# Performance work log

Hardware: AMD Instinct MI355X
Metric: run time of the kernel (lower is better)

Reference implementation:

```python
import jax, jax.numpy as jnp
import numpy as np

N_M = 100000  # musicians
N_T = 100000  # tracks
E = 400000
D = 128


def _sage(x_src, x_dst, edge, W_l, b_l, W_r, n_dst):
    """PyG SAGEConv: lin_l(mean_{j in N(i)} x_src[j]) + lin_r(x_dst[i])."""
    src, dst = edge[0], edge[1]
    msg = x_src[src]                                   # [E, D] gather
    agg = jax.ops.segment_sum(msg, dst, num_segments=n_dst)
    cnt = jax.ops.segment_sum(jnp.ones((edge.shape[1],), x_src.dtype), dst,
                              num_segments=n_dst)
    agg = agg / jnp.maximum(cnt, 1.0)[:, None]         # mean aggregation
    return agg @ W_l.T + b_l + x_dst @ W_r.T


def setup_inputs() -> dict:
    key = jax.random.key(0)
    ks = jax.random.split(key, 7)
    scale = 0.05
    return {
        "x_m": jax.random.normal(ks[0], (N_M, D), jnp.float32),
        "x_t": jax.random.normal(ks[1], (N_T, D), jnp.float32),
        "Wl": jax.random.normal(ks[2], (3, 2, D, D), jnp.float32) * scale,
        "bl": jnp.zeros((3, 2, D), jnp.float32),
        "Wr": jax.random.normal(ks[3], (3, 2, D, D), jnp.float32) * scale,
        "edge_mt": jax.random.randint(ks[4], (2, E), 0, N_T, jnp.int32).astype(jnp.int64),
        "edge_tm": jax.random.randint(ks[5], (2, E), 0, N_M, jnp.int32).astype(jnp.int64),
    }


def reference(x_m, x_t, Wl, bl, Wr, edge_mt, edge_tm):
    # 3 HeteroConv(SAGEConv) layers; dropout=0.0 is identity.
    for layer in range(3):
        # edge type 0: musician -plays_on-> track  (dst = track)
        new_t = _sage(x_m, x_t, edge_mt, Wl[layer, 0], bl[layer, 0], Wr[layer, 0], N_T)
        # edge type 1: track -features-> musician  (dst = musician)
        new_m = _sage(x_t, x_m, edge_tm, Wl[layer, 1], bl[layer, 1], Wr[layer, 1], N_M)
        if layer < 2:
            new_m = jax.nn.relu(new_m)
            new_t = jax.nn.relu(new_t)
        x_m, x_t = new_m, new_t
    return x_m, x_t
```

## Files before the change

### kernel.cpp

```cpp
#include <hip/hip_runtime.h>
#include <hip/hip_bf16.h>

typedef __bf16 bf16_t;
typedef __attribute__((ext_vector_type(4))) __bf16 bf16x4;
typedef __attribute__((ext_vector_type(8))) __bf16 bf16x8;
typedef __attribute__((ext_vector_type(4))) float f32x4;

#define DIM 128

__device__ __forceinline__ void gl_lds16(const void* g, void* l) {
    __builtin_amdgcn_global_load_lds(
        (const __attribute__((address_space(1))) unsigned int*)g,
        (__attribute__((address_space(3))) unsigned int*)l, 16, 0, 0);
}

__global__ void prep_weights(const float* __restrict__ Wl, const float* __restrict__ Wr,
                             bf16_t* __restrict__ Wc) {
    int idx = blockIdx.x * blockDim.x + threadIdx.x;
    if (idx >= 6 * 128 * 256) return;
    int k = idx & 255;
    int n = (idx >> 8) & 127;
    int s = idx >> 15;
    float v;
    if (k < 128) v = Wl[((size_t)s * 128 + n) * 128 + k];
    else         v = Wr[((size_t)s * 128 + n) * 128 + (k - 128)];
    Wc[idx] = (bf16_t)v;
}

__global__ void count_edges2(const int* __restrict__ dA, int* __restrict__ cA,
                             const int* __restrict__ dB, int* __restrict__ cB, int E) {
    int i = blockIdx.x * blockDim.x + threadIdx.x;
    if (i < E) atomicAdd(&cA[dA[i]], 1);
    else if (i < 2 * E) atomicAdd(&cB[dB[i - E]], 1);
}

__global__ __launch_bounds__(256) void scan_local(const int* __restrict__ cnt,
                                                  int* __restrict__ partial,
                                                  int* __restrict__ blocksum, int M) {
    __shared__ int sdata[256];
    int i = blockIdx.x * 256 + threadIdx.x;
    int v = (i < M) ? cnt[i] : 0;
    sdata[threadIdx.x] = v;
    __syncthreads();
    for (int off = 1; off < 256; off <<= 1) {
        int t = (threadIdx.x >= off) ? sdata[threadIdx.x - off] : 0;
        __syncthreads();
        sdata[threadIdx.x] += t;
        __syncthreads();
    }
    int incl = sdata[threadIdx.x];
    if (i < M) partial[i] = incl - v;
    if (threadIdx.x == 255) blocksum[blockIdx.x] = incl;
}

__global__ __launch_bounds__(256) void scan_blocks(int* __restrict__ blocksum, int NB) {
    __shared__ int sdata[256];
    __shared__ int running;
    if (threadIdx.x == 0) running = 0;
    __syncthreads();
    for (int base = 0; base < NB; base += 256) {
        int i = base + threadIdx.x;
        int v = (i < NB) ? blocksum[i] : 0;
        sdata[threadIdx.x] = v;
        __syncthreads();
        for (int off = 1; off < 256; off <<= 1) {
            int t = (threadIdx.x >= off) ? sdata[threadIdx.x - off] : 0;
            __syncthreads();
            sdata[threadIdx.x] += t;
            __syncthreads();
        }
        int incl = sdata[threadIdx.x];
        int r = running;
        __syncthreads();
        if (i < NB) blocksum[i] = incl - v + r;
        if (threadIdx.x == 0) running = r + sdata[255];
        __syncthreads();
    }
}

__global__ void add_offsets(const int* __restrict__ partial, const int* __restrict__ blocksum,
                            int* __restrict__ rowstart, int* __restrict__ cursor, int M) {
    int i = blockIdx.x * blockDim.x + threadIdx.x;
    if (i < M) {
        int rs = partial[i] + blocksum[i >> 8];
        rowstart[i] = rs;
        cursor[i] = rs;
    }
}

__global__ void bin_edges2(const int* __restrict__ sA, const int* __restrict__ dA,
                           int* __restrict__ curA, int* __restrict__ csrA,
                           const int* __restrict__ sB, const int* __restrict__ dB,
                           int* __restrict__ curB, int* __restrict__ csrB, int E) {
    int e = blockIdx.x * blockDim.x + threadIdx.x;
    if (e < E) {
        int d = dA[e];
        int pos = atomicAdd(&curA[d], 1);
        csrA[pos] = sA[e];
    } else if (e < 2 * E) {
        int i = e - E;
        int d = dB[i];
        int pos = atomicAdd(&curB[d], 1);
        csrB[pos] = sB[i];
    }
}

__global__ __launch_bounds__(256) void gather2(
    const float* __restrict__ xsA, const int* __restrict__ rsA,
    const int* __restrict__ cnA, const int* __restrict__ csA,
    bf16_t* __restrict__ agA, int MA,
    const float* __restrict__ xsB, const int* __restrict__ rsB,
    const int* __restrict__ cnB, const int* __restrict__ csB,
    bf16_t* __restrict__ agB, int MB) {
    int gw   = (blockIdx.x * 256 + threadIdx.x) >> 6;
    int lane = threadIdx.x & 63;
    int half = lane >> 5;
    int l32  = lane & 31;
    int side = gw & 1;
    int d    = (gw >> 1) * 2 + half;
    const float* xs; const int *rs, *cn, *cs; bf16_t* ag; int M;
    if (side == 0) { xs = xsA; rs = rsA; cn = cnA; cs = csA; ag = agA; M = MA; }
    else           { xs = xsB; rs = rsB; cn = cnB; cs = csB; ag = agB; M = MB; }
    if (d >= M) return;

    int start = rs[d];
    int n = cn[d];
    float4 acc0 = {0.f, 0.f, 0.f, 0.f};
    float4 acc1 = {0.f, 0.f, 0.f, 0.f};
    int k = 0;
    for (; k + 1 < n; k += 2) {
        int s0 = cs[start + k];
        int s1 = cs[start + k + 1];
        float4 v0 = ((const float4*)(xs + (size_t)s0 * DIM))[l32];
        float4 v1 = ((const float4*)(xs + (size_t)s1 * DIM))[l32];
        acc0.x += v0.x; acc0.y += v0.y; acc0.z += v0.z; acc0.w += v0.w;
        acc1.x += v1.x; acc1.y += v1.y; acc1.z += v1.z; acc1.w += v1.w;
    }
    if (k < n) {
        int s = cs[start + k];
        float4 v = ((const float4*)(xs + (size_t)s * DIM))[l32];
        acc0.x += v.x; acc0.y += v.y; acc0.z += v.z; acc0.w += v.w;
    }
    float invn = 1.0f / (float)max(n, 1);
    bf16x4 r;
    r[0] = (bf16_t)((acc0.x + acc1.x) * invn);
    r[1] = (bf16_t)((acc0.y + acc1.y) * invn);
    r[2] = (bf16_t)((acc0.z + acc1.z) * invn);
    r[3] = (bf16_t)((acc0.w + acc1.w) * invn);
    *(bf16x4*)(ag + (size_t)d * DIM + l32 * 4) = r;
}

#define GTILE   32
#define A0BYTES 8192
#define A1BYTES 16384
#define LDSBUF  (A0BYTES + A1BYTES)

template <bool RELU>
__global__ __launch_bounds__(256, 3) void gemm2(
    const bf16_t* __restrict__ A0a, const float* __restrict__ A1a,
    const bf16_t* __restrict__ Wca, const float* __restrict__ ba,
    float* __restrict__ oa, int Ma,
    const bf16_t* __restrict__ A0b, const float* __restrict__ A1b,
    const bf16_t* __restrict__ Wcb, const float* __restrict__ bb,
    float* __restrict__ ob, int Mb) {
    __shared__ char smem[2 * LDSBUF];
    const int tid  = threadIdx.x;
    const int wid  = tid >> 6;
    const int lane = tid & 63;
    const int quad = lane >> 4;
    const int l16  = lane & 15;

    const int side = blockIdx.x & 1;
    const int t0   = blockIdx.x >> 1;
    const int gs   = gridDim.x >> 1;

    const bf16_t* A0; const float* A1; const bf16_t* Wc; const float* bias; float* out; int M;
    if (side == 0) { A0 = A0a; A1 = A1a; Wc = Wca; bias = ba; out = oa; M = Ma; }
    else           { A0 = A0b; A1 = A1b; Wc = Wcb; bias = bb; out = ob; M = Mb; }
    const int nt = (M + GTILE - 1) / GTILE;
    if (t0 >= nt) return;

    bf16x8 breg[2][8];
#pragma unroll
    for (int ct = 0; ct < 2; ++ct)
#pragma unroll
        for (int kt = 0; kt < 8; ++kt)
            breg[ct][kt] = *(const bf16x8*)(
                Wc + (size_t)(wid * 32 + ct * 16 + l16) * 256 + kt * 32 + quad * 8);

    const float bcol0 = bias[wid * 32 + l16];
    const float bcol1 = bias[wid * 32 + 16 + l16];
    const int sw = l16 & 7;

    int a0row[2], a0sc[2];
#pragma unroll
    for (int c = 0; c < 2; ++c) {
        int o  = wid * 2048 + c * 1024 + lane * 16;
        int row = o >> 8;
        int ch  = (o >> 4) & 15;
        a0row[c] = row;
        a0sc[c]  = (ch ^ (row & 7)) * 8;
    }
    int a1row[4], a1sc[4];
#pragma unroll
    for (int c = 0; c < 4; ++c) {
        int o  = wid * 4096 + c * 1024 + lane * 16;
        int row = o >> 9;
        int ch  = (o >> 4) & 31;
        a1row[c] = row;
        a1sc[c]  = (ch ^ (row & 7)) * 4;
    }

    auto STAGE = [&](int b, int t) {
        const int r0 = t * GTILE;
        char* base = smem + b * LDSBUF;
#pragma unroll
        for (int c = 0; c < 2; ++c) {
            int grow = r0 + a0row[c]; if (grow >= M) grow = M - 1;
            gl_lds16(A0 + (size_t)grow * DIM + a0sc[c],
                     base + wid * 2048 + c * 1024);
        }
#pragma unroll
        for (int c = 0; c < 4; ++c) {
            int grow = r0 + a1row[c]; if (grow >= M) grow = M - 1;
            gl_lds16(A1 + (size_t)grow * DIM + a1sc[c],
                     base + A0BYTES + wid * 4096 + c * 1024);
        }
    };

    auto COMPUTE = [&](int b, int t) {
        const int r0 = t * GTILE;
        const char* a0base = smem + b * LDSBUF;
        const char* a1base = a0base + A0BYTES;
        f32x4 acc[2][2];
#pragma unroll
        for (int rt = 0; rt < 2; ++rt) {
            acc[rt][0] = (f32x4){0.f, 0.f, 0.f, 0.f};
            acc[rt][1] = (f32x4){0.f, 0.f, 0.f, 0.f};
        }
#pragma unroll
        for (int rt = 0; rt < 2; ++rt) {
            const int row = rt * 16 + l16;
            bf16x8 alo[4];
#pragma unroll
            for (int kt = 0; kt < 4; ++kt)
                alo[kt] = *(const bf16x8*)(a0base + row * 256 + ((kt * 4 + quad) ^ sw) * 16);
#pragma unroll
            for (int kt = 0; kt < 4; ++kt) {
                acc[rt][0] = __builtin_amdgcn_mfma_f32_16x16x32_bf16(alo[kt], breg[0][kt], acc[rt][0], 0, 0, 0);
                acc[rt][1] = __builtin_amdgcn_mfma_f32_16x16x32_bf16(alo[kt], breg[1][kt], acc[rt][1], 0, 0, 0);
            }
#pragma unroll
            for (int kt = 0; kt < 4; ++kt) {
                const int cc = kt * 8 + quad * 2;
                float4 x0 = *(const float4*)(a1base + row * 512 + ((cc)     ^ sw) * 16);
                float4 x1 = *(const float4*)(a1base + row * 512 + ((cc + 1) ^ sw) * 16);
                bf16x8 ah;
                ah[0] = (bf16_t)x0.x; ah[1] = (bf16_t)x0.y;
                ah[2] = (bf16_t)x0.z; ah[3] = (bf16_t)x0.w;
                ah[4] = (bf16_t)x1.x; ah[5] = (bf16_t)x1.y;
                ah[6] = (bf16_t)x1.z; ah[7] = (bf16_t)x1.w;
                acc[rt][0] = __builtin_amdgcn_mfma_f32_16x16x32_bf16(ah, breg[0][kt + 4], acc[rt][0], 0, 0, 0);
                acc[rt][1] = __builtin_amdgcn_mfma_f32_16x16x32_bf16(ah, breg[1][kt + 4], acc[rt][1], 0, 0, 0);
            }
        }
#pragma unroll
        for (int ct = 0; ct < 2; ++ct) {
            const int col = wid * 32 + ct * 16 + l16;
            const float bv = ct ? bcol1 : bcol0;
#pragma unroll
            for (int rt = 0; rt < 2; ++rt)
#pragma unroll
                for (int r = 0; r < 4; ++r) {
                    int row = r0 + rt * 16 + quad * 4 + r;
                    if (row < M) {
                        float v = acc[rt][ct][r] + bv;
                        if (RELU) v = fmaxf(v, 0.f);
                        out[(size_t)row * DIM + col] = v;
                    }
                }
        }
    };

    STAGE(0, t0);
    int bufi = 0;
    for (int t = t0; t < nt; t += gs, bufi ^= 1) {
        const int nxt = t + gs;
        if (nxt < nt) {
            STAGE(bufi ^ 1, nxt);
            asm volatile("s_waitcnt vmcnt(6)" ::: "memory");
        } else {
            asm volatile("s_waitcnt vmcnt(0)" ::: "memory");
        }
        __builtin_amdgcn_s_barrier();
        COMPUTE(bufi, t);
        __builtin_amdgcn_s_barrier();
        __builtin_amdgcn_sched_barrier(0);
    }
}

extern "C" void kernel_launch(void* const* d_in, const int* in_sizes, int n_in,
                              void* d_out, int out_size, void* d_ws, size_t ws_size,
                              hipStream_t stream) {
    const float* x_m = (const float*)d_in[0];
    const float* x_t = (const float*)d_in[1];
    const float* Wl  = (const float*)d_in[2];
    const float* bl  = (const float*)d_in[3];
    const float* Wr  = (const float*)d_in[4];
    const int* e_mt  = (const int*)d_in[5];
    const int* e_tm  = (const int*)d_in[6];

    const int Mm = in_sizes[0] / DIM;
    const int Mt = in_sizes[1] / DIM;
    const int E  = in_sizes[5] / 2;
    const int NBt = (Mt + 255) / 256;
    const int NBm = (Mm + 255) / 256;

    float* out_m = (float*)d_out;
    float* out_t = (float*)d_out + (size_t)Mm * DIM;

    char* ws = (char*)d_ws;
    size_t off = 0;
    auto alloc = [&](size_t bytes) -> void* {
        void* p = ws + off;
        off += (bytes + 255) & ~(size_t)255;
        return p;
    };
    float*  xm2    = (float*)alloc((size_t)Mm * DIM * 4);
    float*  xt2    = (float*)alloc((size_t)Mt * DIM * 4);
    bf16_t* aggT   = (bf16_t*)alloc((size_t)Mt * DIM * 2);
    bf16_t* aggM   = (bf16_t*)alloc((size_t)Mm * DIM * 2);
    int*    cnt_t  = (int*)alloc((size_t)Mt * 4);
    int*    cnt_m  = (int*)alloc((size_t)Mm * 4);
    int*    rs_t   = (int*)alloc((size_t)Mt * 4);
    int*    rs_m   = (int*)alloc((size_t)Mm * 4);
    int*    cur_tb = (int*)alloc((size_t)Mt * 4);
    int*    cur_mb = (int*)alloc((size_t)Mm * 4);
    int*    partial= (int*)alloc((size_t)((Mm > Mt) ? Mm : Mt) * 4);
    int*    bsum   = (int*)alloc((size_t)((NBt > NBm) ? NBt : NBm) * 4);
    int*    csr_t  = (int*)alloc((size_t)E * 4);
    int*    csr_m  = (int*)alloc((size_t)E * 4);
    bf16_t* Wc     = (bf16_t*)alloc((size_t)6 * 128 * 256 * 2);

    hipMemsetAsync(cnt_t, 0, (size_t)Mt * 4, stream);
    hipMemsetAsync(cnt_m, 0, (size_t)Mm * 4, stream);
    prep_weights<<<(6 * 128 * 256 + 255) / 256, 256, 0, stream>>>(Wl, Wr, Wc);
    count_edges2<<<(2 * E + 255) / 256, 256, 0, stream>>>(e_mt + E, cnt_t, e_tm + E, cnt_m, E);

    scan_local<<<NBt, 256, 0, stream>>>(cnt_t, partial, bsum, Mt);
    scan_blocks<<<1, 256, 0, stream>>>(bsum, NBt);
    add_offsets<<<NBt, 256, 0, stream>>>(partial, bsum, rs_t, cur_tb, Mt);

    scan_local<<<NBm, 256, 0, stream>>>(cnt_m, partial, bsum, Mm);
    scan_blocks<<<1, 256, 0, stream>>>(bsum, NBm);
    add_offsets<<<NBm, 256, 0, stream>>>(partial, bsum, rs_m, cur_mb, Mm);

    bin_edges2<<<(2 * E + 255) / 256, 256, 0, stream>>>(e_mt, e_mt + E, cur_tb, csr_t,
                                                        e_tm, e_tm + E, cur_mb, csr_m, E);

    const int wT = (Mt + 1) / 2, wM = (Mm + 1) / 2;
    const int gwaves = 2 * ((wT > wM) ? wT : wM);
    const int gblocks = (gwaves + 3) / 4;

    int GG = 768;
    {
        int ntT = (Mt + GTILE - 1) / GTILE, ntM = (Mm + GTILE - 1) / GTILE;
        int need = 2 * ((ntT > ntM) ? ntT : ntM);
        if (GG > need) GG = need;
        GG &= ~1;
        if (GG < 2) GG = 2;
    }

    const float* cm = x_m;
    const float* ct = x_t;
    for (int layer = 0; layer < 3; ++layer) {
        float *nxt_m, *nxt_t;
        if (layer == 1) { nxt_m = xm2;   nxt_t = xt2;   }
        else            { nxt_m = out_m; nxt_t = out_t; }
        const float* biasT = bl + ((size_t)layer * 2 + 0) * DIM;
        const float* biasM = bl + ((size_t)layer * 2 + 1) * DIM;
        const bf16_t* WcT = Wc + ((size_t)layer * 2 + 0) * 128 * 256;
        const bf16_t* WcM = Wc + ((size_t)layer * 2 + 1) * 128 * 256;

        gather2<<<gblocks, 256, 0, stream>>>(cm, rs_t, cnt_t, csr_t, aggT, Mt,
                                             ct, rs_m, cnt_m, csr_m, aggM, Mm);
        if (layer < 2)
            gemm2<true ><<<GG, 256, 0, stream>>>(aggT, ct, WcT, biasT, nxt_t, Mt,
                                                 aggM, cm, WcM, biasM, nxt_m, Mm);
        else
            gemm2<false><<<GG, 256, 0, stream>>>(aggT, ct, WcT, biasT, nxt_t, Mt,
                                                 aggM, cm, WcM, biasM, nxt_m, Mm);

        cm = nxt_m;
        ct = nxt_t;
    }
}
```

Measured before the change: 594.5 us.

## Merge CSR preprocessing launches and batch 8 neighbor gathers per iteration

Combines weight prep with edge counting, and runs the two scans and offset passes for both edge types in single launches. This cuts the preprocessing kernel count from eight to four and removes serialization between them, at the cost of separate partial and blocksum buffers per edge type. The aggregation loop now issues 8 index loads and 8 row gathers per iteration, with clamped indices and zero weights for the tail. This raises memory-level parallelism but adds redundant loads for low-degree nodes, which are common here at an average degree of about 4.

```diff
diff --git a/kernel.cpp b/kernel.cpp
--- a/kernel.cpp
+++ b/kernel.cpp
@@ -14,31 +14,40 @@
         (__attribute__((address_space(3))) unsigned int*)l, 16, 0, 0);
 }
 
-__global__ void prep_weights(const float* __restrict__ Wl, const float* __restrict__ Wr,
-                             bf16_t* __restrict__ Wc) {
-    int idx = blockIdx.x * blockDim.x + threadIdx.x;
-    if (idx >= 6 * 128 * 256) return;
-    int k = idx & 255;
-    int n = (idx >> 8) & 127;
-    int s = idx >> 15;
-    float v;
-    if (k < 128) v = Wl[((size_t)s * 128 + n) * 128 + k];
-    else         v = Wr[((size_t)s * 128 + n) * 128 + (k - 128)];
-    Wc[idx] = (bf16_t)v;
-}
-
-__global__ void count_edges2(const int* __restrict__ dA, int* __restrict__ cA,
-                             const int* __restrict__ dB, int* __restrict__ cB, int E) {
-    int i = blockIdx.x * blockDim.x + threadIdx.x;
-    if (i < E) atomicAdd(&cA[dA[i]], 1);
-    else if (i < 2 * E) atomicAdd(&cB[dB[i - E]], 1);
-}
-
-__global__ __launch_bounds__(256) void scan_local(const int* __restrict__ cnt,
-                                                  int* __restrict__ partial,
-                                                  int* __restrict__ blocksum, int M) {
+__global__ void prep_count(const float* __restrict__ Wl, const float* __restrict__ Wr,
+                           bf16_t* __restrict__ Wc,
+                           const int* __restrict__ dA, int* __restrict__ cA,
+                           const int* __restrict__ dB, int* __restrict__ cB,
+                           int E, int PB) {
+    int blk = blockIdx.x;
+    if (blk < PB) {
+        int idx = blk * 256 + threadIdx.x;
+        if (idx >= 6 * 128 * 256) return;
+        int k = idx & 255;
+        int n = (idx >> 8) & 127;
+        int s = idx >> 15;
+        float v;
+        if (k < 128) v = Wl[((size_t)s * 128 + n) * 128 + k];
+        else         v = Wr[((size_t)s * 128 + n) * 128 + (k - 128)];
+        Wc[idx] = (bf16_t)v;
+    } else {
+        int i = (blk - PB) * 256 + threadIdx.x;
+        if (i < E) atomicAdd(&cA[dA[i]], 1);
+        else if (i < 2 * E) atomicAdd(&cB[dB[i - E]], 1);
+    }
+}
+
+__global__ __launch_bounds__(256) void scan_local2(
+    const int* __restrict__ cntA, int* __restrict__ partA, int* __restrict__ bsumA,
+    int MA, int NBA,
+    const int* __restrict__ cntB, int* __restrict__ partB, int* __restrict__ bsumB,
+    int MB) {
+    int blk = blockIdx.x;
+    const int* cnt; int* partial; int* blocksum; int M; int b;
+    if (blk < NBA) { cnt = cntA; partial = partA; blocksum = bsumA; M = MA; b = blk; }
+    else           { cnt = cntB; partial = partB; blocksum = bsumB; M = MB; b = blk - NBA; }
     __shared__ int sdata[256];
-    int i = blockIdx.x * 256 + threadIdx.x;
+    int i = b * 256 + threadIdx.x;
     int v = (i < M) ? cnt[i] : 0;
     sdata[threadIdx.x] = v;
     __syncthreads();
@@ -50,10 +59,13 @@
     }
     int incl = sdata[threadIdx.x];
     if (i < M) partial[i] = incl - v;
-    if (threadIdx.x == 255) blocksum[blockIdx.x] = incl;
-}
-
-__global__ __launch_bounds__(256) void scan_blocks(int* __restrict__ blocksum, int NB) {
+    if (threadIdx.x == 255) blocksum[b] = incl;
+}
+
+__global__ __launch_bounds__(256) void scan_blocks2(int* __restrict__ bsA, int NA,
+                                                    int* __restrict__ bsB, int NBcnt) {
+    int* blocksum = blockIdx.x ? bsB : bsA;
+    int NB = blockIdx.x ? NBcnt : NA;
     __shared__ int sdata[256];
     __shared__ int running;
     if (threadIdx.x == 0) running = 0;
@@ -78,9 +90,16 @@
     }
 }
 
-__global__ void add_offsets(const int* __restrict__ partial, const int* __restrict__ blocksum,
-                            int* __restrict__ rowstart, int* __restrict__ cursor, int M) {
-    int i = blockIdx.x * blockDim.x + threadIdx.x;
+__global__ __launch_bounds__(256) void add_offsets2(
+    const int* __restrict__ pA, const int* __restrict__ bsA,
+    int* __restrict__ rsA, int* __restrict__ curA, int MA, int NBA,
+    const int* __restrict__ pB, const int* __restrict__ bsB,
+    int* __restrict__ rsB, int* __restrict__ curB, int MB) {
+    int blk = blockIdx.x;
+    const int *partial, *blocksum; int *rowstart, *cursor; int M, b;
+    if (blk < NBA) { partial = pA; blocksum = bsA; rowstart = rsA; cursor = curA; M = MA; b = blk; }
+    else           { partial = pB; blocksum = bsB; rowstart = rsB; cursor = curB; M = MB; b = blk - NBA; }
+    int i = b * 256 + threadIdx.x;
     if (i < M) {
         int rs = partial[i] + blocksum[i >> 8];
         rowstart[i] = rs;
@@ -127,19 +146,26 @@
     int n = cn[d];
     float4 acc0 = {0.f, 0.f, 0.f, 0.f};
     float4 acc1 = {0.f, 0.f, 0.f, 0.f};
-    int k = 0;
-    for (; k + 1 < n; k += 2) {
-        int s0 = cs[start + k];
-        int s1 = cs[start + k + 1];
-        float4 v0 = ((const float4*)(xs + (size_t)s0 * DIM))[l32];
-        float4 v1 = ((const float4*)(xs + (size_t)s1 * DIM))[l32];
-        acc0.x += v0.x; acc0.y += v0.y; acc0.z += v0.z; acc0.w += v0.w;
-        acc1.x += v1.x; acc1.y += v1.y; acc1.z += v1.z; acc1.w += v1.w;
-    }
-    if (k < n) {
-        int s = cs[start + k];
-        float4 v = ((const float4*)(xs + (size_t)s * DIM))[l32];
-        acc0.x += v.x; acc0.y += v.y; acc0.z += v.z; acc0.w += v.w;
+    for (int k = 0; k < n; k += 8) {
+        int sv[8];
+#pragma unroll
+        for (int j = 0; j < 8; ++j) {
+            int kk = k + j;
+            sv[j] = cs[start + min(kk, n - 1)];
+        }
+        float4 vv[8];
+#pragma unroll
+        for (int j = 0; j < 8; ++j)
+            vv[j] = ((const float4*)(xs + (size_t)sv[j] * DIM))[l32];
+#pragma unroll
+        for (int j = 0; j < 8; j += 2) {
+            float w0 = (k + j     < n) ? 1.f : 0.f;
+            float w1 = (k + j + 1 < n) ? 1.f : 0.f;
+            acc0.x += vv[j].x * w0; acc0.y += vv[j].y * w0;
+            acc0.z += vv[j].z * w0; acc0.w += vv[j].w * w0;
+            acc1.x += vv[j + 1].x * w1; acc1.y += vv[j + 1].y * w1;
+            acc1.z += vv[j + 1].z * w1; acc1.w += vv[j + 1].w * w1;
+        }
     }
     float invn = 1.0f / (float)max(n, 1);
     bf16x4 r;
@@ -336,25 +362,26 @@
     int*    rs_m   = (int*)alloc((size_t)Mm * 4);
     int*    cur_tb = (int*)alloc((size_t)Mt * 4);
     int*    cur_mb = (int*)alloc((size_t)Mm * 4);
-    int*    partial= (int*)alloc((size_t)((Mm > Mt) ? Mm : Mt) * 4);
-    int*    bsum   = (int*)alloc((size_t)((NBt > NBm) ? NBt : NBm) * 4);
+    int*    part_t = (int*)alloc((size_t)Mt * 4);
+    int*    part_m = (int*)alloc((size_t)Mm * 4);
+    int*    bsum_t = (int*)alloc((size_t)NBt * 4);
+    int*    bsum_m = (int*)alloc((size_t)NBm * 4);
     int*    csr_t  = (int*)alloc((size_t)E * 4);
     int*    csr_m  = (int*)alloc((size_t)E * 4);
     bf16_t* Wc     = (bf16_t*)alloc((size_t)6 * 128 * 256 * 2);
 
     hipMemsetAsync(cnt_t, 0, (size_t)Mt * 4, stream);
     hipMemsetAsync(cnt_m, 0, (size_t)Mm * 4, stream);
-    prep_weights<<<(6 * 128 * 256 + 255) / 256, 256, 0, stream>>>(Wl, Wr, Wc);
-    count_edges2<<<(2 * E + 255) / 256, 256, 0, stream>>>(e_mt + E, cnt_t, e_tm + E, cnt_m, E);
-
-    scan_local<<<NBt, 256, 0, stream>>>(cnt_t, partial, bsum, Mt);
-    scan_blocks<<<1, 256, 0, stream>>>(bsum, NBt);
-    add_offsets<<<NBt, 256, 0, stream>>>(partial, bsum, rs_t, cur_tb, Mt);
-
-    scan_local<<<NBm, 256, 0, stream>>>(cnt_m, partial, bsum, Mm);
-    scan_blocks<<<1, 256, 0, stream>>>(bsum, NBm);
-    add_offsets<<<NBm, 256, 0, stream>>>(partial, bsum, rs_m, cur_mb, Mm);
-
+
+    const int PB = (6 * 128 * 256 + 255) / 256;
+    const int CB = (2 * E + 255) / 256;
+    prep_count<<<PB + CB, 256, 0, stream>>>(Wl, Wr, Wc, e_mt + E, cnt_t, e_tm + E, cnt_m, E, PB);
+
+    scan_local2<<<NBt + NBm, 256, 0, stream>>>(cnt_t, part_t, bsum_t, Mt, NBt,
+                                               cnt_m, part_m, bsum_m, Mm);
+    scan_blocks2<<<2, 256, 0, stream>>>(bsum_t, NBt, bsum_m, NBm);
+    add_offsets2<<<NBt + NBm, 256, 0, stream>>>(part_t, bsum_t, rs_t, cur_tb, Mt, NBt,
+                                                part_m, bsum_m, rs_m, cur_mb, Mm);
     bin_edges2<<<(2 * E + 255) / 256, 256, 0, stream>>>(e_mt, e_mt + E, cur_tb, csr_t,
                                                         e_tm, e_tm + E, cur_mb, csr_m, E);
 
```

After: 567.2 us. 1.05x faster.
